# Performance work log

Measured on AMD Instinct MI355X. Metric: run time of the kernel, lower is better.

Reference implementation:

```python
import jax, jax.numpy as jnp
import numpy as np
from jax import lax

# ---- model dims (match init_kwargs) ----
D = 2048        # hidden_size
HD = 128        # head_dim
HQ = 16         # num_q_heads (= expanded_num_heads)
HK = 8          # num_k_heads = num_v_heads
CONV = 4        # conv_size
CHUNK = 64      # chunk_size
NUM_ITER = 30   # chebyshev iterations
RIDGE = 0.02
EPS = 1e-6


def setup_inputs() -> dict:
    key = jax.random.key(0)
    ks = jax.random.split(key, 20)
    s = 0.02
    inp = {}
    inp['hidden_states'] = jax.random.normal(ks[0], (1, 1024, D), jnp.float32)
    inp['Wq'] = jax.random.normal(ks[1], (D, HQ * HD), jnp.float32) * s
    inp['Wk'] = jax.random.normal(ks[2], (D, HK * HD), jnp.float32) * s
    inp['Wv'] = jax.random.normal(ks[3], (D, HK * HD), jnp.float32) * s
    inp['conv_q'] = jax.random.normal(ks[4], (HQ * HD, CONV), jnp.float32) * 0.3
    inp['conv_k'] = jax.random.normal(ks[5], (HK * HD, CONV), jnp.float32) * 0.3
    inp['conv_v'] = jax.random.normal(ks[6], (HK * HD, CONV), jnp.float32) * 0.3
    inp['Wa'] = jax.random.normal(ks[7], (D, HQ), jnp.float32) * s
    # A_log = log(Uniform(0,16)) as in torch init
    inp['A_log'] = jnp.log(jax.random.uniform(ks[8], (HQ,), jnp.float32, 1e-3, 16.0))
    # dt_bias = inverse-softplus of dt ~ LogUniform(1e-3, 1e-1)
    dt = jnp.exp(jax.random.uniform(ks[9], (HQ,), jnp.float32) * (np.log(0.1) - np.log(0.001)) + np.log(0.001))
    dt = jnp.clip(dt, 1e-4, None)
    inp['dt_bias'] = dt + jnp.log(-jnp.expm1(-dt))
    inp['Wb'] = jax.random.normal(ks[10], (D, HQ), jnp.float32) * s
    inp['bb'] = jnp.zeros((HQ,), jnp.float32)
    inp['Walpha'] = jax.random.normal(ks[11], (D, HQ), jnp.float32) * s
    inp['balpha'] = jnp.zeros((HQ,), jnp.float32)
    inp['Wg'] = jax.random.normal(ks[12], (D, HQ * HD), jnp.float32) * s
    inp['norm_w'] = jnp.ones((HD,), jnp.float32)
    inp['Wo'] = jax.random.normal(ks[13], (HQ * HD, D), jnp.float32) * s
    return inp


def short_conv(x, w):
    # causal depthwise conv1d (kernel=CONV) + silu; x:[B,L,C], w:[C,K]
    K = w.shape[1]
    L = x.shape[1]
    xp = jnp.pad(x, ((0, 0), (K - 1, 0), (0, 0)))
    y = sum(xp[:, j:j + L, :] * w[:, j] for j in range(K))
    return jax.nn.silu(y)


def cheb_solve(A, b, lmin, lmax, num_iter):
    # Chebyshev semi-iteration for SPD A x = b, eigenvalue bounds [lmin, lmax].
    # A, b: [..., d, d]; lmin scalar; lmax: [..., 1, 1]
    theta = (lmax + lmin) / 2.0
    delta = (lmax - lmin) / 2.0
    sigma1 = theta / delta
    x = jnp.zeros_like(b)
    r = b
    rho = 1.0 / sigma1
    dvec = r / theta
    def body(carry, _):
        x, r, dvec, rho = carry
        x = x + dvec
        r = r - jnp.einsum('...de,...ef->...df', A, dvec)
        rho_n = 1.0 / (2.0 * sigma1 - rho)
        dvec = rho_n * rho * dvec + (2.0 * rho_n / delta) * r
        return (x, r, dvec, rho_n), None
    (x, _, _, _), _ = lax.scan(body, (x, r, dvec, rho), None, length=num_iter)
    return x


def reference(hidden_states, Wq, Wk, Wv, conv_q, conv_k, conv_v, Wa, A_log, dt_bias,
              Wb, bb, Walpha, balpha, Wg, norm_w, Wo):
    x = hidden_states
    B, L, _ = x.shape
    H, Hk, d, C = HQ, HK, HD, CHUNK
    Nc = L // C

    # projections + short causal convs with silu
    q = short_conv(x @ Wq, conv_q).reshape(B, L, H, d) * (d ** -0.5)  # gla rescale
    k = short_conv(x @ Wk, conv_k).reshape(B, L, Hk, d)
    v = short_conv(x @ Wv, conv_v).reshape(B, L, Hk, d)
    grp = H // Hk
    k = jnp.repeat(k, grp, axis=2)  # GQA expand: (h g) ordering
    v = jnp.repeat(v, grp, axis=2)

    # gates
    glog = -jnp.exp(A_log) * jax.nn.softplus(x @ Wa + dt_bias)   # [B,L,H], log forgetting gate <= 0
    beta = jax.nn.sigmoid(x @ Wb + bb)                           # [B,L,H]
    alpha = jax.nn.sigmoid(x @ Walpha + balpha)                  # [B,L,H]

    # chunk: [B,H,Nc,C,...]
    def ch(t):
        return t.reshape(B, Nc, C, H, -1).transpose(0, 3, 1, 2, 4)
    qc, kc, vc = ch(q), ch(k), ch(v)
    glc = glog.reshape(B, Nc, C, H).transpose(0, 3, 1, 2)   # [B,H,Nc,C]
    bc = beta.reshape(B, Nc, C, H).transpose(0, 3, 1, 2)

    cs = jnp.cumsum(glc, axis=-1)         # inclusive cumulative log-decay within chunk
    G = cs[..., -1]                        # total chunk decay [B,H,Nc]
    w_end = jnp.exp(G[..., None] - cs) * bc
    dHn = jnp.einsum('bhnc,bhncd,bhnce->bhnde', w_end, kc, kc)  # gram increment (forgetting_gate_kk)
    dBn = jnp.einsum('bhnc,bhncd,bhnce->bhnde', w_end, kc, vc)  # kv increment
    dg = jnp.exp(G)

    # inter-chunk state recurrence (scan over chunks)
    def step(carry, inp):
        Hs, Bs = carry
        g_n, dH_n, dB_n = inp
        out = (Hs, Bs)  # state at chunk START
        Hs = g_n[..., None, None] * Hs + dH_n
        Bs = g_n[..., None, None] * Bs + dB_n
        return (Hs, Bs), out
    init = (jnp.zeros((B, H, d, d), x.dtype), jnp.zeros((B, H, d, d), x.dtype))
    inputs = (dg.transpose(2, 0, 1), dHn.transpose(2, 0, 1, 3, 4), dBn.transpose(2, 0, 1, 3, 4))
    _, (H0, B0) = lax.scan(step, init, inputs)  # [Nc,B,H,d,d]

    # ridge-regularized Kalman solve per chunk via Chebyshev
    A = H0 + RIDGE * jnp.eye(d, dtype=x.dtype)
    lmax = jnp.trace(A, axis1=-2, axis2=-1)[..., None, None]  # trace >= lambda_max for SPD
    X = cheb_solve(A, B0, RIDGE, lmax, NUM_ITER)              # [Nc,B,H,d,d]
    Xc = X.transpose(1, 2, 0, 3, 4)                           # [B,H,Nc,d,d]

    # inter-chunk readout (through solved state)
    o_inter = jnp.exp(cs)[..., None] * jnp.einsum('bhncd,bhnde->bhnce', qc, Xc)
    # intra-chunk causal gated attention
    diff = cs[..., :, None] - cs[..., None, :]                # [B,H,Nc,C,C]
    mask = jnp.tril(jnp.ones((C, C), bool))
    dmat = jnp.exp(jnp.where(mask, diff, -1e30))
    scores = jnp.einsum('bhncd,bhnjd->bhncj', qc, kc) * dmat * bc[..., None, :]
    o_intra = jnp.einsum('bhncj,bhnjd->bhncd', scores, vc)

    o = (o_inter + o_intra).transpose(0, 2, 3, 1, 4).reshape(B, L, H, d)
    o = o + alpha[..., None] * v   # alpha connection (residual value path)

    # gated RMSNorm + output projection
    g_out = (x @ Wg).reshape(B, L, H, d)
    o = o * lax.rsqrt(jnp.mean(o * o, axis=-1, keepdims=True) + EPS) * norm_w
    o = o * jax.nn.silu(g_out)
    return o.reshape(B, L, H * d) @ Wo
```

## Files before the change

kernel.cpp:

```cpp
#include <hip/hip_runtime.h>
#include <math.h>


#define LSEQ 1024
#define DM   2048
#define NHQ  16
#define NHK  8
#define HDIM 128
#define NCH  16
#define CSZ  64

typedef __attribute__((ext_vector_type(8))) short short8;
typedef __attribute__((ext_vector_type(4))) float floatx4;

__device__ __forceinline__ unsigned short f2bf(float f) {
  unsigned int u = __float_as_uint(f);
  u += 0x7fffu + ((u >> 16) & 1u);
  return (unsigned short)(u >> 16);
}
__device__ __forceinline__ float bf2f(unsigned short u) {
  return __uint_as_float(((unsigned int)u) << 16);
}

__device__ __forceinline__ void tcast_fat(
    const float* __restrict__ W, unsigned short* __restrict__ Wt,
    int K, int N, int bn, int bk, int tid, float* __restrict__ t) {
  int k0 = bk * 128, n0 = bn * 64;
#pragma unroll
  for (int i = 0; i < 8; ++i) {
    int u = tid + i * 256;
    int r = u >> 4, c4 = u & 15;
    float4 v = *(const float4*)(W + (size_t)(k0 + r) * N + n0 + c4 * 4);
    float* dst = t + r * 65 + c4 * 4;
    dst[0] = v.x; dst[1] = v.y; dst[2] = v.z; dst[3] = v.w;
  }
  __syncthreads();
#pragma unroll
  for (int i = 0; i < 4; ++i) {
    int u2 = tid + i * 256;
    int klow = u2 & 7, nlow = (u2 >> 3) & 7;
    int khigh = (u2 >> 6) & 1, nhigh = (u2 >> 7) & 7;
    int k8 = (klow + khigh * 8) * 8;
    int nn = nlow + nhigh * 8;
    unsigned short o8[8];
#pragma unroll
    for (int j = 0; j < 8; ++j) o8[j] = f2bf(t[(k8 + j) * 65 + nn]);
    *(uint4*)(Wt + (size_t)(n0 + nn) * K + k0 + k8) = *(uint4*)o8;
  }
}

__global__ __launch_bounds__(256) void prep_kernel(
    const float* __restrict__ x, const float* __restrict__ Wq,
    const float* __restrict__ Wk, const float* __restrict__ Wv,
    const float* __restrict__ Wg, unsigned short* __restrict__ xb16,
    unsigned short* __restrict__ WtAll,
    const float* __restrict__ Wa, const float* __restrict__ Wbeta,
    const float* __restrict__ Wal, const float* __restrict__ A_log,
    const float* __restrict__ dtb, const float* __restrict__ bbv,
    const float* __restrict__ balv, float* __restrict__ glog,
    float* __restrict__ beta, float* __restrict__ alpha) {
  __shared__ float smem[128 * 65];
  int b = blockIdx.x, tid = threadIdx.x;
  if (b < 1024) {
    float* xr = smem;
    float* part = smem + 2048;
    int ts = b;
    for (int i = tid; i < 512; i += 256)
      ((float4*)xr)[i] = ((const float4*)(x + (size_t)ts * 2048))[i];
    __syncthreads();
    int o = tid >> 2, p = tid & 3;
    float s = 0.f;
    if (o < 48) {
      const float* W = (o < 16) ? Wa : (o < 32) ? Wbeta : Wal;
      int h = o & 15;
      int k0 = p * 512;
      for (int k = k0; k < k0 + 512; ++k) s = fmaf(xr[k], W[k * 16 + h], s);
    }
    part[tid] = s;
    __syncthreads();
    if (o < 48 && p == 0) {
      float dot = part[tid] + part[tid + 1] + part[tid + 2] + part[tid + 3];
      int h = o & 15;
      if (o < 16) {
        float za = dot + dtb[h];
        float sp = fmaxf(za, 0.f) + log1pf(expf(-fabsf(za)));
        glog[ts * 16 + h] = -expf(A_log[h]) * sp;
      } else if (o < 32) {
        beta[ts * 16 + h] = 1.f / (1.f + expf(-(dot + bbv[h])));
      } else {
        alpha[ts * 16 + h] = 1.f / (1.f + expf(-(dot + balv[h])));
      }
    }
  } else if (b < 2560) {
    int r = b - 1024;
    if (r < 512) {
      tcast_fat(Wq, WtAll, 2048, 2048, r & 31, r >> 5, tid, smem);
    } else if (r < 768) {
      int q = r - 512;
      tcast_fat(Wk, WtAll + (size_t)2048 * 2048, 2048, 1024, q & 15, q >> 4,
                tid, smem);
    } else if (r < 1024) {
      int q = r - 768;
      tcast_fat(Wv, WtAll + (size_t)3072 * 2048, 2048, 1024, q & 15, q >> 4,
                tid, smem);
    } else {
      int q = r - 1024;
      tcast_fat(Wg, WtAll + (size_t)4096 * 2048, 2048, 2048, q & 31, q >> 5,
                tid, smem);
    }
  } else {
    int i0 = (b - 2560) * 1024 + tid;
#pragma unroll
    for (int i = 0; i < 4; ++i) {
      int idx = i0 + i * 256;
      float4 v = ((const float4*)x)[idx];
      ushort4 u;
      u.x = f2bf(v.x); u.y = f2bf(v.y); u.z = f2bf(v.z); u.w = f2bf(v.w);
      ((ushort4*)xb16)[idx] = u;
    }
  }
}

__global__ __launch_bounds__(256) void gemm_bf16(
    const unsigned short* __restrict__ A, const unsigned short* __restrict__ Bt,
    float* __restrict__ C, int M, int N, int K) {
  __shared__ unsigned short As[128 * 72];
  __shared__ unsigned short Bs[64 * 72];
  int tid = threadIdx.x;
  int wave = tid >> 6, lane = tid & 63;
  int ln = lane & 15, hi = lane >> 4;
  int wm = wave & 1, wn = wave >> 1;
  int m0 = blockIdx.y * 128, n0 = blockIdx.x * 64;

  floatx4 acc[4][2];
#pragma unroll
  for (int mt = 0; mt < 4; ++mt)
#pragma unroll
    for (int nt = 0; nt < 2; ++nt) acc[mt][nt] = (floatx4)(0.f);

  for (int k0 = 0; k0 < K; k0 += 64) {
#pragma unroll
    for (int g = 0; g < 4; ++g) {
      int l = tid + g * 256;
      int m = l >> 3, go = l & 7;
      uint4 v = *(const uint4*)(A + (size_t)(m0 + m) * K + k0 + go * 8);
      *(uint4*)(As + m * 72 + go * 8) = v;
    }
#pragma unroll
    for (int g = 0; g < 2; ++g) {
      int l = tid + g * 256;
      int n = l >> 3, go = l & 7;
      uint4 v = *(const uint4*)(Bt + (size_t)(n0 + n) * K + k0 + go * 8);
      *(uint4*)(Bs + n * 72 + go * 8) = v;
    }
    __syncthreads();
#pragma unroll
    for (int kb = 0; kb < 2; ++kb) {
      short8 a[4], b[2];
#pragma unroll
      for (int mt = 0; mt < 4; ++mt)
        a[mt] = *(const short8*)(As + (wm * 64 + mt * 16 + ln) * 72 + kb * 32 + hi * 8);
#pragma unroll
      for (int nt = 0; nt < 2; ++nt)
        b[nt] = *(const short8*)(Bs + (wn * 32 + nt * 16 + ln) * 72 + kb * 32 + hi * 8);
#pragma unroll
      for (int mt = 0; mt < 4; ++mt)
#pragma unroll
        for (int nt = 0; nt < 2; ++nt)
          acc[mt][nt] = __builtin_amdgcn_mfma_f32_16x16x32_bf16(
              a[mt], b[nt], acc[mt][nt], 0, 0, 0);
    }
    __syncthreads();
  }
#pragma unroll
  for (int mt = 0; mt < 4; ++mt)
#pragma unroll
    for (int nt = 0; nt < 2; ++nt) {
      int col = n0 + wn * 32 + nt * 16 + ln;
      int rowb = m0 + wm * 64 + mt * 16 + hi * 4;
#pragma unroll
      for (int r = 0; r < 4; ++r)
        C[(size_t)(rowb + r) * N + col] = acc[mt][nt][r];
    }
}

__device__ __forceinline__ float conv_core(
    const float* __restrict__ xin, const float* __restrict__ w,
    int idx, int instride, int nch, float scale) {
  int t = idx / nch, ch = idx - t * nch;
  float acc = 0.f;
#pragma unroll
  for (int j = 0; j < 4; ++j) {
    int tt = t + j - 3;
    float xv = (tt >= 0) ? xin[(size_t)tt * instride + ch] : 0.f;
    acc = fmaf(xv, w[ch * 4 + j], acc);
  }
  return acc / (1.f + expf(-acc)) * scale;
}

__global__ __launch_bounds__(256) void conv_all(
    const float* __restrict__ xall, const float* __restrict__ convq,
    const float* __restrict__ convk, const float* __restrict__ convv,
    unsigned short* __restrict__ qs16, float* __restrict__ ks2,
    unsigned short* __restrict__ ks16, float* __restrict__ vs2,
    const float* __restrict__ glog, const float* __restrict__ beta,
    float* __restrict__ cs, float* __restrict__ wend) {
  int b = blockIdx.x, tid = threadIdx.x;
  if (b < 8192) {
    int idx = b * 256 + tid;
    qs16[idx] = f2bf(conv_core(xall, convq, idx, 6144, 2048,
                               0.08838834764831845f));
  } else if (b < 12288) {
    int idx = (b - 8192) * 256 + tid;
    float v = conv_core(xall + 2048, convk, idx, 6144, 1024, 1.0f);
    ks2[idx] = v;
    ks16[idx] = f2bf(v);
  } else if (b < 16384) {
    int idx = (b - 12288) * 256 + tid;
    vs2[idx] = conv_core(xall + 3072, convv, idx, 6144, 1024, 1.0f);
  } else {
    int idx = tid;
    int n = idx & 15;
    float acc = 0.f;
    for (int c = 0; c < CSZ; ++c) {
      acc += glog[(n * CSZ + c) * NHQ + (idx >> 4)];
      cs[idx * CSZ + c] = acc;
    }
    float G = acc;
    for (int c = 0; c < CSZ; ++c) {
      wend[idx * CSZ + c] =
          expf(G - cs[idx * CSZ + c]) * beta[(n * CSZ + c) * NHQ + (idx >> 4)];
    }
  }
}

__global__ __launch_bounds__(256) void dhb_kernel(
    const float* __restrict__ ks, const float* __restrict__ vs,
    const float* __restrict__ wend, float* __restrict__ dH,
    float* __restrict__ dB, unsigned short* __restrict__ vT16) {
  __shared__ uint4 smem4[4096];
  int bid = blockIdx.x;
  int tid = threadIdx.x;

  if (bid >= 256) {
    float* t = (float*)smem4;
    int b = bid - 256;
    size_t gbase = ((size_t)(b >> 3)) * 65536 + ((size_t)(b & 7)) * 128;
#pragma unroll
    for (int g = 0; g < 8; ++g) {
      int i = tid + g * 256;
      int c = i >> 5, e4 = i & 31;
      float4 v = *(const float4*)(vs + gbase + (size_t)c * 1024 + e4 * 4);
      t[c * 132 + e4 * 4 + 0] = v.x;
      t[c * 132 + e4 * 4 + 1] = v.y;
      t[c * 132 + e4 * 4 + 2] = v.z;
      t[c * 132 + e4 * 4 + 3] = v.w;
    }
    __syncthreads();
    int e = tid >> 1, half = tid & 1;
    size_t obase = ((size_t)b << 13) + (size_t)e * 64 + half * 32;
#pragma unroll
    for (int cc = 0; cc < 8; ++cc) {
      int c0 = half * 32 + cc * 4;
      ushort4 u;
      u.x = f2bf(t[(c0 + 0) * 132 + e]);
      u.y = f2bf(t[(c0 + 1) * 132 + e]);
      u.z = f2bf(t[(c0 + 2) * 132 + e]);
      u.w = f2bf(t[(c0 + 3) * 132 + e]);
      *(ushort4*)(vT16 + obase + cc * 4) = u;
    }
    return;
  }

  unsigned short (*skF)[8192] = (unsigned short (*)[8192])smem4;
  unsigned short (*svF)[8192] =
      (unsigned short (*)[8192])((unsigned short*)smem4 + 16384);
  int h = bid >> 4, n = bid & 15;
  int hk = h >> 1;

#pragma unroll
  for (int p = 0; p < 4; ++p) {
    int t2 = tid + p * 256;
    int c0 = (t2 >> 7) << 3;
    int e = t2 & 127;
    int base = ((e >> 4) * 2 + (c0 >> 5)) * 512 +
               ((c0 & 31) >> 3) * 128 + (e & 15) * 8;
    unsigned short kh[8], kl[8], vh[8], vl[8];
#pragma unroll
    for (int j = 0; j < 8; ++j) {
      int c = c0 + j;
      float s = sqrtf(wend[bid * 64 + c]);
      size_t g = (size_t)(n * 64 + c) * 1024 + hk * 128 + e;
      float kf = s * ks[g];
      float vf = s * vs[g];
      unsigned short khh = f2bf(kf);
      kh[j] = khh; kl[j] = f2bf(kf - bf2f(khh));
      unsigned short vhh = f2bf(vf);
      vh[j] = vhh; vl[j] = f2bf(vf - bf2f(vhh));
    }
    *(uint4*)(&skF[0][base]) = *(uint4*)kh;
    *(uint4*)(&skF[1][base]) = *(uint4*)kl;
    *(uint4*)(&svF[0][base]) = *(uint4*)vh;
    *(uint4*)(&svF[1][base]) = *(uint4*)vl;
  }
  __syncthreads();

  int w = tid >> 6, lane = tid & 63;
  int ln = lane & 15, hi = lane >> 4;

  short8 ah[2][2], al[2][2];
#pragma unroll
  for (int mti = 0; mti < 2; ++mti) {
    int mt = w * 2 + mti;
#pragma unroll
    for (int ct = 0; ct < 2; ++ct) {
      ah[mti][ct] = *(const short8*)(&skF[0][((mt * 2 + ct) * 64 + lane) * 8]);
      al[mti][ct] = *(const short8*)(&skF[1][((mt * 2 + ct) * 64 + lane) * 8]);
    }
  }

  size_t gb = (size_t)bid << 14;
#pragma unroll
  for (int which = 0; which < 2; ++which) {
    const unsigned short (*BF)[8192] = which ? svF : skF;
    float* outp = which ? dB : dH;
#pragma unroll
    for (int nt = 0; nt < 8; ++nt) {
      floatx4 a0 = (floatx4)(0.f), a1 = (floatx4)(0.f);
#pragma unroll
      for (int ct = 0; ct < 2; ++ct) {
        short8 bh = *(const short8*)(&BF[0][((nt * 2 + ct) * 64 + lane) * 8]);
        short8 bl = *(const short8*)(&BF[1][((nt * 2 + ct) * 64 + lane) * 8]);
        a0 = __builtin_amdgcn_mfma_f32_16x16x32_bf16(ah[0][ct], bh, a0, 0, 0, 0);
        a0 = __builtin_amdgcn_mfma_f32_16x16x32_bf16(ah[0][ct], bl, a0, 0, 0, 0);
        a0 = __builtin_amdgcn_mfma_f32_16x16x32_bf16(al[0][ct], bh, a0, 0, 0, 0);
        a1 = __builtin_amdgcn_mfma_f32_16x16x32_bf16(ah[1][ct], bh, a1, 0, 0, 0);
        a1 = __builtin_amdgcn_mfma_f32_16x16x32_bf16(ah[1][ct], bl, a1, 0, 0, 0);
        a1 = __builtin_amdgcn_mfma_f32_16x16x32_bf16(al[1][ct], bh, a1, 0, 0, 0);
      }
      int e = nt * 16 + ln;
#pragma unroll
      for (int rg = 0; rg < 4; ++rg) {
        int d0 = (w * 2 + 0) * 16 + hi * 4 + rg;
        int d1 = (w * 2 + 1) * 16 + hi * 4 + rg;
        outp[gb + (size_t)d0 * 128 + e] = a0[rg];
        outp[gb + (size_t)d1 * 128 + e] = a1[rg];
      }
    }
  }
}

__global__ __launch_bounds__(256) void scan_kernel(
    float* __restrict__ dH, float* __restrict__ dB,
    const float* __restrict__ cs) {
  int idx = blockIdx.x * 256 + threadIdx.x;
  int h = idx >> 14, de = idx & 16383;
  float Hs = 0.f, Bs = 0.f;
  bool diag = ((de % 129) == 0);
#pragma unroll 1
  for (int n = 0; n < NCH; ++n) {
    size_t off = ((size_t)(h * 16 + n) << 14) + de;
    float dh = dH[off], db = dB[off];
    dH[off] = diag ? (Hs + 0.02f) : Hs;
    dB[off] = Bs;
    float g = expf(cs[(h * 16 + n) * CSZ + (CSZ - 1)]);
    Hs = fmaf(g, Hs, dh);
    Bs = fmaf(g, Bs, db);
  }
}

__global__ __launch_bounds__(256) void afrag_kernel(
    float* __restrict__ Aall, float* __restrict__ traces) {
  int bid = blockIdx.x;
  float* Ag = Aall + ((size_t)bid << 14);
  __shared__ float As[16384];
  int tid = threadIdx.x;
  for (int i = tid; i < 4096; i += 256)
    ((float4*)As)[i] = ((const float4*)Ag)[i];
  __syncthreads();
  if (tid < 64) {
    float tv = As[tid * 129] + As[(tid + 64) * 129];
#pragma unroll
    for (int off = 32; off; off >>= 1) tv += __shfl_down(tv, off);
    if (tid == 0) traces[bid] = tv;
  }
  unsigned short* Ah = (unsigned short*)Ag;
  unsigned short* Al = Ah + 16384;
#pragma unroll
  for (int c8 = 0; c8 < 8; ++c8) {
    int s0 = tid * 64 + c8 * 8;
    int frag = s0 >> 9, mlane = (s0 >> 3) & 63;
    int m = ((frag >> 2) << 4) + (mlane & 15);
    int k = ((frag & 3) << 5) + ((mlane >> 4) << 3);
    unsigned short hi[8], lo[8];
#pragma unroll
    for (int j = 0; j < 8; ++j) {
      float a = As[m * 128 + k + j];
      unsigned short h = f2bf(a);
      hi[j] = h;
      lo[j] = f2bf(a - bf2f(h));
    }
    *(uint4*)(Ah + s0) = *(uint4*)hi;
    *(uint4*)(Al + s0) = *(uint4*)lo;
  }
}

__global__ __launch_bounds__(512, 4) void cheb_kernel(
    const unsigned short* __restrict__ Afrag, const float* __restrict__ traces,
    float* __restrict__ Ball) {
  int bm = blockIdx.x >> 2;
  int cb = blockIdx.x & 3;
  const unsigned short* __restrict__ Ah = Afrag + ((size_t)bm << 15);
  float* __restrict__ Bg = Ball + ((size_t)bm << 14);
  __shared__ unsigned short dT[2][4096];
  int tid = threadIdx.x;
  int w = tid >> 6, lane = tid & 63;
  int ln = lane & 15, q = lane >> 4;

  float lmax = traces[bm];
  const float lmin = 0.02f;
  float theta = 0.5f * (lmax + lmin);
  float delta = 0.5f * (lmax - lmin);
  float sigma1 = theta / delta;
  float rho = delta / theta;
  float invtheta = 1.f / theta;

  short8 afr[4][2];
#pragma unroll
  for (int kt = 0; kt < 4; ++kt) {
    afr[kt][0] = *(const short8*)(Ah + (((w * 4 + kt) * 64 + lane) << 3));
    afr[kt][1] = *(const short8*)(Ah + 16384 + (((w * 4 + kt) * 64 + lane) << 3));
  }

  int wrA = ((w >> 1) * 64 + (((w & 1) * 2 + (q >> 1)) * 16 + ln)) * 8 +
            ((q & 1) << 2);

  float xx[2][4], rr[2][4], dd[2][4];
#pragma unroll
  for (int nt = 0; nt < 2; ++nt) {
    int nn = cb * 32 + nt * 16 + ln;
    ushort4 pack;
    unsigned short* pp = (unsigned short*)&pack;
#pragma unroll
    for (int rg = 0; rg < 4; ++rg) {
      float b = Bg[(w * 16 + q * 4 + rg) * 128 + nn];
      rr[nt][rg] = b;
      xx[nt][rg] = 0.f;
      unsigned short dq = f2bf(b * invtheta);
      dd[nt][rg] = bf2f(dq);
      pp[rg] = dq;
    }
    *(ushort4*)(&dT[0][nt * 2048 + wrA]) = pack;
  }
  __syncthreads();

#pragma unroll 1
  for (int it = 0; it < 30; ++it) {
    const unsigned short* dTr = dT[it & 1];
    unsigned short* dTw = dT[(it & 1) ^ 1];
    floatx4 acc[2];
    acc[0] = (floatx4)(0.f);
    acc[1] = (floatx4)(0.f);
#pragma unroll
    for (int kt = 0; kt < 4; ++kt) {
      short8 df0 = *(const short8*)(dTr + (((0 * 4 + kt) * 64 + lane) << 3));
      short8 df1 = *(const short8*)(dTr + (((1 * 4 + kt) * 64 + lane) << 3));
      acc[0] = __builtin_amdgcn_mfma_f32_16x16x32_bf16(afr[kt][0], df0, acc[0], 0, 0, 0);
      acc[0] = __builtin_amdgcn_mfma_f32_16x16x32_bf16(afr[kt][1], df0, acc[0], 0, 0, 0);
      acc[1] = __builtin_amdgcn_mfma_f32_16x16x32_bf16(afr[kt][0], df1, acc[1], 0, 0, 0);
      acc[1] = __builtin_amdgcn_mfma_f32_16x16x32_bf16(afr[kt][1], df1, acc[1], 0, 0, 0);
    }
    float rho_n = 1.f / (2.f * sigma1 - rho);
    float c1s = rho_n * rho;
    float c2s = 2.f * rho_n / delta;
#pragma unroll
    for (int nt = 0; nt < 2; ++nt) {
      ushort4 pack;
      unsigned short* pp = (unsigned short*)&pack;
#pragma unroll
      for (int rg = 0; rg < 4; ++rg) {
        xx[nt][rg] += dd[nt][rg];
        rr[nt][rg] -= acc[nt][rg];
        float dn = fmaf(c1s, dd[nt][rg], c2s * rr[nt][rg]);
        unsigned short dq = f2bf(dn);
        dd[nt][rg] = bf2f(dq);
        pp[rg] = dq;
      }
      *(ushort4*)(&dTw[nt * 2048 + wrA]) = pack;
    }
    rho = rho_n;
    __syncthreads();
  }

  unsigned short* Xf = (unsigned short*)Bg;
#pragma unroll
  for (int nt = 0; nt < 2; ++nt) {
    ushort4 h4, l4;
    unsigned short* hp = (unsigned short*)&h4;
    unsigned short* lp = (unsigned short*)&l4;
#pragma unroll
    for (int rg = 0; rg < 4; ++rg) {
      float xv = xx[nt][rg];
      unsigned short h = f2bf(xv);
      hp[rg] = h;
      lp[rg] = f2bf(xv - bf2f(h));
    }
    int lhi = nt * 2048 + wrA;
    int llo = lhi + 4096;
    *(ushort4*)(Xf + ((lhi >> 6) * 256 + cb * 64 + (lhi & 63))) = h4;
    *(ushort4*)(Xf + ((llo >> 6) * 256 + cb * 64 + (llo & 63))) = l4;
  }
}

__global__ __launch_bounds__(256) void attn_kernel(
    const unsigned short* __restrict__ q16, const unsigned short* __restrict__ k16,
    const unsigned short* __restrict__ vT16, const unsigned short* __restrict__ Xf,
    const float* __restrict__ vs, const float* __restrict__ cs,
    const float* __restrict__ beta, const float* __restrict__ alpha,
    float* __restrict__ o) {
  int bid = blockIdx.x;
  int h = bid >> 4, n = bid & 15;
  int hk = h >> 1;
  __shared__ unsigned short qb[64 * 136];
  __shared__ unsigned short kb[64 * 136];
  __shared__ unsigned short Sb[64 * 72];
  __shared__ float csL[64], ecsL[64], betaL[64], alphaL[64];
  int tid = threadIdx.x;
  int w = tid >> 6, lane = tid & 63;
  int ln = lane & 15, hi = lane >> 4;

  {
    size_t qgb = (((size_t)(n * 64)) * 16 + h) * 128;
    size_t kgb = (((size_t)(n * 64)) * 8 + hk) * 128;
#pragma unroll
    for (int g = 0; g < 4; ++g) {
      int i = tid + g * 256;
      int c = i >> 4, ch = i & 15;
      *(uint4*)(qb + c * 136 + ch * 8) =
          *(const uint4*)(q16 + qgb + (size_t)c * 2048 + ch * 8);
      *(uint4*)(kb + c * 136 + ch * 8) =
          *(const uint4*)(k16 + kgb + (size_t)c * 1024 + ch * 8);
    }
    if (tid < 64) {
      float cv = cs[bid * 64 + tid];
      csL[tid] = cv;
      ecsL[tid] = expf(cv);
      betaL[tid] = beta[(n * 64 + tid) * 16 + h];
      alphaL[tid] = alpha[(n * 64 + tid) * 16 + h];
    }
  }
  __syncthreads();

  short8 aq[4];
#pragma unroll
  for (int dt = 0; dt < 4; ++dt)
    aq[dt] = *(const short8*)(qb + (w * 16 + ln) * 136 + dt * 32 + hi * 8);

  const unsigned short* Xb = Xf + ((size_t)bid << 15);
  floatx4 acc[8];
#pragma unroll
  for (int et = 0; et < 8; ++et) {
    int cbq = et >> 1, ntl = et & 1;
    floatx4 a = (floatx4)(0.f);
#pragma unroll
    for (int dt = 0; dt < 4; ++dt) {
      int lhi = ntl * 2048 + dt * 512 + lane * 8;
      int llo = lhi + 4096;
      short8 xh = *(const short8*)(Xb + ((lhi >> 6) * 256 + cbq * 64 + (lhi & 63)));
      short8 xl = *(const short8*)(Xb + ((llo >> 6) * 256 + cbq * 64 + (llo & 63)));
      a = __builtin_amdgcn_mfma_f32_16x16x32_bf16(aq[dt], xh, a, 0, 0, 0);
      a = __builtin_amdgcn_mfma_f32_16x16x32_bf16(aq[dt], xl, a, 0, 0, 0);
    }
    acc[et] = a;
  }
#pragma unroll
  for (int et = 0; et < 8; ++et)
#pragma unroll
    for (int rg = 0; rg < 4; ++rg)
      acc[et][rg] *= ecsL[w * 16 + hi * 4 + rg];

#pragma unroll
  for (int jt = 0; jt < 4; ++jt) {
    if (jt <= w) {
      floatx4 s = (floatx4)(0.f);
#pragma unroll
      for (int dt = 0; dt < 4; ++dt) {
        short8 bk = *(const short8*)(kb + (jt * 16 + ln) * 136 + dt * 32 + hi * 8);
        s = __builtin_amdgcn_mfma_f32_16x16x32_bf16(aq[dt], bk, s, 0, 0, 0);
      }
      int j = jt * 16 + ln;
      float csj = csL[j], bj = betaL[j];
#pragma unroll
      for (int rg = 0; rg < 4; ++rg) {
        int c = w * 16 + hi * 4 + rg;
        float v = (j <= c) ? s[rg] * expf(csL[c] - csj) * bj : 0.f;
        Sb[c * 72 + j] = f2bf(v);
      }
    } else {
#pragma unroll
      for (int rg = 0; rg < 4; ++rg)
        Sb[(w * 16 + hi * 4 + rg) * 72 + jt * 16 + ln] = 0;
    }
  }

  const unsigned short* vTb = vT16 + ((size_t)(n * 8 + hk) << 13);
#pragma unroll
  for (int et = 0; et < 8; ++et) {
#pragma unroll
    for (int kt = 0; kt < 2; ++kt) {
      short8 as = *(const short8*)(Sb + (w * 16 + ln) * 72 + kt * 32 + hi * 8);
      short8 bv = *(const short8*)(vTb + (et * 16 + ln) * 64 + kt * 32 + hi * 8);
      acc[et] = __builtin_amdgcn_mfma_f32_16x16x32_bf16(as, bv, acc[et], 0, 0, 0);
    }
  }

#pragma unroll
  for (int et = 0; et < 8; ++et) {
#pragma unroll
    for (int rg = 0; rg < 4; ++rg) {
      int c = w * 16 + hi * 4 + rg, e = et * 16 + ln;
      size_t oaddr = (((size_t)(n * 64 + c)) * 16 + h) * 128 + e;
      size_t vaddr = (((size_t)(n * 64 + c)) * 8 + hk) * 128 + e;
      o[oaddr] = acc[et][rg] + alphaL[c] * vs[vaddr];
    }
  }
}

__global__ __launch_bounds__(256) void rmso_kernel(
    const float* __restrict__ o, const float* __restrict__ xall,
    const float* __restrict__ norm_w, unsigned short* __restrict__ onorm,
    const float* __restrict__ Wo, unsigned short* __restrict__ WtWo) {
  __shared__ float t[128 * 65];
  int b = blockIdx.x, tid = threadIdx.x;
  if (b < 512) {
    tcast_fat(Wo, WtWo, 2048, 2048, b & 31, b >> 5, tid, t);
  } else {
    int bb = b - 512;
    int wave = tid >> 6, lane = tid & 63;
    int row = bb * 4 + wave;
    size_t base = (size_t)row * HDIM;
    size_t gbase = (size_t)(row >> 4) * 6144 + 4096 + (size_t)(row & 15) * HDIM;
    float v0 = o[base + lane], v1 = o[base + lane + 64];
    float ss = fmaf(v0, v0, v1 * v1);
#pragma unroll
    for (int off = 32; off; off >>= 1) ss += __shfl_down(ss, off);
    ss = __shfl(ss, 0);
    float rinv = rsqrtf(ss * (1.f / 128.f) + 1e-6f);
    float g0 = xall[gbase + lane], g1 = xall[gbase + lane + 64];
    float s0 = g0 / (1.f + expf(-g0));
    float s1 = g1 / (1.f + expf(-g1));
    onorm[base + lane]      = f2bf(v0 * rinv * norm_w[lane] * s0);
    onorm[base + lane + 64] = f2bf(v1 * rinv * norm_w[lane + 64] * s1);
  }
}

extern "C" void kernel_launch(void* const* d_in, const int* in_sizes, int n_in,
                              void* d_out, int out_size, void* d_ws,
                              size_t ws_size, hipStream_t stream) {
  (void)in_sizes; (void)n_in; (void)out_size; (void)ws_size;
  const float* x      = (const float*)d_in[0];
  const float* Wq     = (const float*)d_in[1];
  const float* Wk     = (const float*)d_in[2];
  const float* Wv     = (const float*)d_in[3];
  const float* convq  = (const float*)d_in[4];
  const float* convk  = (const float*)d_in[5];
  const float* convv  = (const float*)d_in[6];
  const float* Wa     = (const float*)d_in[7];
  const float* A_log  = (const float*)d_in[8];
  const float* dtb    = (const float*)d_in[9];
  const float* Wb     = (const float*)d_in[10];
  const float* bbv    = (const float*)d_in[11];
  const float* Wal    = (const float*)d_in[12];
  const float* balv   = (const float*)d_in[13];
  const float* Wg     = (const float*)d_in[14];
  const float* norm_w = (const float*)d_in[15];
  const float* Wo     = (const float*)d_in[16];
  float* out = (float*)d_out;

  float* p = (float*)d_ws;
  float* xall  = p; p += 6291456;
  float* qslot = p; p += 2097152;
  float* ks2   = p; p += 1048576;
  float* vs2   = p; p += 1048576;
  float* ob    = p; p += 2097152;
  float* glog  = p; p += 16384;
  float* beta  = p; p += 16384;
  float* alpha = p; p += 16384;
  float* csb   = p; p += 16384;
  float* wend  = p; p += 16384;
  float* traces= p; p += 16384;
  float* dHn   = p; p += 4194304;
  float* dBn   = p; p += 4194304;
  unsigned short* xb16 = (unsigned short*)p; p += 1048576;

  unsigned short* qs16 = (unsigned short*)qslot;
  unsigned short* ks16 = qs16 + 2097152;
  unsigned short* vT16 = ks16 + 1048576;
  unsigned short* WtAll = (unsigned short*)dHn;
  unsigned short* WtWo  = (unsigned short*)ks2;
  unsigned short* onorm16 = xb16;

  dim3 blk(256);
  prep_kernel<<<3072, blk, 0, stream>>>(x, Wq, Wk, Wv, Wg, xb16, WtAll,
                                        Wa, Wb, Wal, A_log, dtb, bbv, balv,
                                        glog, beta, alpha);
  gemm_bf16<<<dim3(96, 8), blk, 0, stream>>>(xb16, WtAll, xall, 1024, 6144, 2048);
  conv_all<<<16385, blk, 0, stream>>>(xall, convq, convk, convv,
                                      qs16, ks2, ks16, vs2,
                                      glog, beta, csb, wend);
  dhb_kernel<<<384, blk, 0, stream>>>(ks2, vs2, wend, dHn, dBn, vT16);
  scan_kernel<<<1024, blk, 0, stream>>>(dHn, dBn, csb);
  afrag_kernel<<<256, blk, 0, stream>>>(dHn, traces);
  cheb_kernel<<<1024, dim3(512), 0, stream>>>((unsigned short*)dHn, traces, dBn);
  attn_kernel<<<256, blk, 0, stream>>>(qs16, ks16, vT16, (unsigned short*)dBn,
                                       vs2, csb, beta, alpha, ob);
  rmso_kernel<<<4608, blk, 0, stream>>>(ob, xall, norm_w, onorm16, Wo, WtWo);
  gemm_bf16<<<dim3(32, 8), blk, 0, stream>>>(onorm16, WtWo, out, 1024, 2048, 2048);
}
```

Baseline: 420.8 us.

## Split Chebyshev solve into narrower column blocks with 256-thread workgroups

The Chebyshev kernel now runs 2048 workgroups of 256 threads, each owning a 16-column slice of the right-hand side, instead of 1024 workgroups of 512 threads owning 32 columns. Each wave holds two row tiles of A, so it needs one LDS fragment load per k-step and synchronises a smaller workgroup each iteration. The output fragment layout is changed to match, and the attention kernel's X loads are rewritten for the new layout. In exchange, A fragments are loaded from global memory twice as often in total, and each wave holds more A registers.

```diff
diff --git a/kernel.cpp b/kernel.cpp
--- a/kernel.cpp
+++ b/kernel.cpp
@@ -405,14 +405,15 @@
   }
 }
 
-__global__ __launch_bounds__(512, 4) void cheb_kernel(
+__global__ __launch_bounds__(256, 4) void cheb_kernel(
     const unsigned short* __restrict__ Afrag, const float* __restrict__ traces,
     float* __restrict__ Ball) {
-  int bm = blockIdx.x >> 2;
-  int cb = blockIdx.x & 3;
+  int bid = blockIdx.x;
+  int bm = bid & 255;
+  int cb = bid >> 8;
   const unsigned short* __restrict__ Ah = Afrag + ((size_t)bm << 15);
   float* __restrict__ Bg = Ball + ((size_t)bm << 14);
-  __shared__ unsigned short dT[2][4096];
+  __shared__ unsigned short dT[2][2048];
   int tid = threadIdx.x;
   int w = tid >> 6, lane = tid & 63;
   int ln = lane & 15, q = lane >> 4;
@@ -425,32 +426,37 @@
   float rho = delta / theta;
   float invtheta = 1.f / theta;
 
-  short8 afr[4][2];
-#pragma unroll
-  for (int kt = 0; kt < 4; ++kt) {
-    afr[kt][0] = *(const short8*)(Ah + (((w * 4 + kt) * 64 + lane) << 3));
-    afr[kt][1] = *(const short8*)(Ah + 16384 + (((w * 4 + kt) * 64 + lane) << 3));
-  }
-
-  int wrA = ((w >> 1) * 64 + (((w & 1) * 2 + (q >> 1)) * 16 + ln)) * 8 +
-            ((q & 1) << 2);
+  short8 afr[2][4][2];
+#pragma unroll
+  for (int mt = 0; mt < 2; ++mt)
+#pragma unroll
+    for (int kt = 0; kt < 4; ++kt) {
+      int f = (w * 2 + mt) * 4 + kt;
+      afr[mt][kt][0] = *(const short8*)(Ah + ((f * 64 + lane) << 3));
+      afr[mt][kt][1] = *(const short8*)(Ah + 16384 + ((f * 64 + lane) << 3));
+    }
+
+  int wrB[2];
+#pragma unroll
+  for (int mt = 0; mt < 2; ++mt)
+    wrB[mt] = w * 512 + (((mt * 2 + (q >> 1)) & 3) * 16 + ln) * 8 +
+              ((q & 1) << 2);
 
   float xx[2][4], rr[2][4], dd[2][4];
 #pragma unroll
-  for (int nt = 0; nt < 2; ++nt) {
-    int nn = cb * 32 + nt * 16 + ln;
+  for (int mt = 0; mt < 2; ++mt) {
     ushort4 pack;
     unsigned short* pp = (unsigned short*)&pack;
 #pragma unroll
     for (int rg = 0; rg < 4; ++rg) {
-      float b = Bg[(w * 16 + q * 4 + rg) * 128 + nn];
-      rr[nt][rg] = b;
-      xx[nt][rg] = 0.f;
+      float b = Bg[(w * 32 + mt * 16 + q * 4 + rg) * 128 + cb * 16 + ln];
+      rr[mt][rg] = b;
+      xx[mt][rg] = 0.f;
       unsigned short dq = f2bf(b * invtheta);
-      dd[nt][rg] = bf2f(dq);
+      dd[mt][rg] = bf2f(dq);
       pp[rg] = dq;
     }
-    *(ushort4*)(&dT[0][nt * 2048 + wrA]) = pack;
+    *(ushort4*)(&dT[0][wrB[mt]]) = pack;
   }
   __syncthreads();
 
@@ -458,35 +464,32 @@
   for (int it = 0; it < 30; ++it) {
     const unsigned short* dTr = dT[it & 1];
     unsigned short* dTw = dT[(it & 1) ^ 1];
-    floatx4 acc[2];
-    acc[0] = (floatx4)(0.f);
-    acc[1] = (floatx4)(0.f);
+    floatx4 a0 = (floatx4)(0.f), a1 = (floatx4)(0.f);
 #pragma unroll
     for (int kt = 0; kt < 4; ++kt) {
-      short8 df0 = *(const short8*)(dTr + (((0 * 4 + kt) * 64 + lane) << 3));
-      short8 df1 = *(const short8*)(dTr + (((1 * 4 + kt) * 64 + lane) << 3));
-      acc[0] = __builtin_amdgcn_mfma_f32_16x16x32_bf16(afr[kt][0], df0, acc[0], 0, 0, 0);
-      acc[0] = __builtin_amdgcn_mfma_f32_16x16x32_bf16(afr[kt][1], df0, acc[0], 0, 0, 0);
-      acc[1] = __builtin_amdgcn_mfma_f32_16x16x32_bf16(afr[kt][0], df1, acc[1], 0, 0, 0);
-      acc[1] = __builtin_amdgcn_mfma_f32_16x16x32_bf16(afr[kt][1], df1, acc[1], 0, 0, 0);
+      short8 df = *(const short8*)(dTr + kt * 512 + lane * 8);
+      a0 = __builtin_amdgcn_mfma_f32_16x16x32_bf16(afr[0][kt][0], df, a0, 0, 0, 0);
+      a0 = __builtin_amdgcn_mfma_f32_16x16x32_bf16(afr[0][kt][1], df, a0, 0, 0, 0);
+      a1 = __builtin_amdgcn_mfma_f32_16x16x32_bf16(afr[1][kt][0], df, a1, 0, 0, 0);
+      a1 = __builtin_amdgcn_mfma_f32_16x16x32_bf16(afr[1][kt][1], df, a1, 0, 0, 0);
     }
     float rho_n = 1.f / (2.f * sigma1 - rho);
     float c1s = rho_n * rho;
     float c2s = 2.f * rho_n / delta;
 #pragma unroll
-    for (int nt = 0; nt < 2; ++nt) {
+    for (int mt = 0; mt < 2; ++mt) {
       ushort4 pack;
       unsigned short* pp = (unsigned short*)&pack;
 #pragma unroll
       for (int rg = 0; rg < 4; ++rg) {
-        xx[nt][rg] += dd[nt][rg];
-        rr[nt][rg] -= acc[nt][rg];
-        float dn = fmaf(c1s, dd[nt][rg], c2s * rr[nt][rg]);
+        xx[mt][rg] += dd[mt][rg];
+        rr[mt][rg] -= mt ? a1[rg] : a0[rg];
+        float dn = fmaf(c1s, dd[mt][rg], c2s * rr[mt][rg]);
         unsigned short dq = f2bf(dn);
-        dd[nt][rg] = bf2f(dq);
+        dd[mt][rg] = bf2f(dq);
         pp[rg] = dq;
       }
-      *(ushort4*)(&dTw[nt * 2048 + wrA]) = pack;
+      *(ushort4*)(&dTw[wrB[mt]]) = pack;
     }
     rho = rho_n;
     __syncthreads();
@@ -494,21 +497,21 @@
 
   unsigned short* Xf = (unsigned short*)Bg;
 #pragma unroll
-  for (int nt = 0; nt < 2; ++nt) {
+  for (int mt = 0; mt < 2; ++mt) {
     ushort4 h4, l4;
     unsigned short* hp = (unsigned short*)&h4;
     unsigned short* lp = (unsigned short*)&l4;
 #pragma unroll
     for (int rg = 0; rg < 4; ++rg) {
-      float xv = xx[nt][rg];
+      float xv = xx[mt][rg];
       unsigned short h = f2bf(xv);
       hp[rg] = h;
       lp[rg] = f2bf(xv - bf2f(h));
     }
-    int lhi = nt * 2048 + wrA;
-    int llo = lhi + 4096;
-    *(ushort4*)(Xf + ((lhi >> 6) * 256 + cb * 64 + (lhi & 63))) = h4;
-    *(ushort4*)(Xf + ((llo >> 6) * 256 + cb * 64 + (llo & 63))) = l4;
+    int lhi = wrB[mt];
+    int llo = lhi + 2048;
+    *(ushort4*)(Xf + ((lhi >> 5) << 8) + (cb << 5) + (lhi & 31)) = h4;
+    *(ushort4*)(Xf + ((llo >> 5) << 8) + (cb << 5) + (llo & 31)) = l4;
   }
 }
 
@@ -560,14 +563,12 @@
   floatx4 acc[8];
 #pragma unroll
   for (int et = 0; et < 8; ++et) {
-    int cbq = et >> 1, ntl = et & 1;
     floatx4 a = (floatx4)(0.f);
 #pragma unroll
     for (int dt = 0; dt < 4; ++dt) {
-      int lhi = ntl * 2048 + dt * 512 + lane * 8;
-      int llo = lhi + 4096;
-      short8 xh = *(const short8*)(Xb + ((lhi >> 6) * 256 + cbq * 64 + (lhi & 63)));
-      short8 xl = *(const short8*)(Xb + ((llo >> 6) * 256 + cbq * 64 + (llo & 63)));
+      int base = ((dt * 16 + (lane >> 2)) << 8) + (et << 5) + ((lane & 3) << 3);
+      short8 xh = *(const short8*)(Xb + base);
+      short8 xl = *(const short8*)(Xb + base + 16384);
       a = __builtin_amdgcn_mfma_f32_16x16x32_bf16(aq[dt], xh, a, 0, 0, 0);
       a = __builtin_amdgcn_mfma_f32_16x16x32_bf16(aq[dt], xl, a, 0, 0, 0);
     }
@@ -711,7 +712,7 @@
   dhb_kernel<<<384, blk, 0, stream>>>(ks2, vs2, wend, dHn, dBn, vT16);
   scan_kernel<<<1024, blk, 0, stream>>>(dHn, dBn, csb);
   afrag_kernel<<<256, blk, 0, stream>>>(dHn, traces);
-  cheb_kernel<<<1024, dim3(512), 0, stream>>>((unsigned short*)dHn, traces, dBn);
+  cheb_kernel<<<2048, blk, 0, stream>>>((unsigned short*)dHn, traces, dBn);
   attn_kernel<<<256, blk, 0, stream>>>(qs16, ks16, vT16, (unsigned short*)dBn,
                                        vs2, csb, beta, alpha, ob);
   rmso_kernel<<<4608, blk, 0, stream>>>(ob, xall, norm_w, onorm16, Wo, WtWo);
```

Measured after the change: 420.4 us. No clear change (-0.1%).
